# Kernel tuning notes

Measured on AMD Instinct MI355X. Metric: run time of the kernel, lower is better.

The kernel has to match this reference:

```python
import jax, jax.numpy as jnp
import numpy as np

DN = ('NCHW', 'OIHW', 'NCHW')
A, NC = 3, 80  # num_anchors, num_classes


def conv(x, w, b, pad=1):
    y = jax.lax.conv_general_dilated(x, w, (1, 1), [(pad, pad), (pad, pad)], dimension_numbers=DN)
    return y + b[None, :, None, None]


def up2(x):
    return jnp.repeat(jnp.repeat(x, 2, axis=2), 2, axis=3)


def gen_anchors():
    # AnchorGenerator: sizes per level, 3 aspect ratios, 1 scale, stride=2**(i+3)
    sizes = [32.0, 64.0, 128.0]
    ars = [0.5, 1.0, 2.0]
    hw = [(64, 64), (32, 32), (16, 16)]
    out = []
    for i, ((h, w), bs) in enumerate(zip(hw, sizes)):
        stride = 2.0 ** (i + 3)
        base = np.array([[-bs * np.sqrt(a) / 2, -bs / np.sqrt(a) / 2,
                          bs * np.sqrt(a) / 2, bs / np.sqrt(a) / 2] for a in ars], dtype=np.float32)
        sx = np.arange(w, dtype=np.float32) * stride
        sy = np.arange(h, dtype=np.float32) * stride
        yy, xx = np.meshgrid(sy, sx, indexing='ij')  # torch.meshgrid default 'ij'
        shifts = np.stack([xx.ravel(), yy.ravel(), xx.ravel(), yy.ravel()], axis=1)
        anc = (base[None, :, :] + shifts[:, None, :]).reshape(-1, 4)
        out.append(anc)
    return jnp.asarray(np.concatenate(out, axis=0))


def setup_inputs() -> dict:
    key = jax.random.key(0)
    ks = jax.random.split(key, 32)
    def w(k, o, i, kh, kw):
        return jax.random.normal(k, (o, i, kh, kw), jnp.float32) * 0.02
    B = 8
    inp = {
        'feat3': jax.random.normal(ks[0], (B, 512, 64, 64), jnp.float32),
        'feat4': jax.random.normal(ks[1], (B, 1024, 32, 32), jnp.float32),
        'feat5': jax.random.normal(ks[2], (B, 2048, 16, 16), jnp.float32),
        # FPN lateral 1x1 convs
        'lw0': w(ks[3], 256, 512, 1, 1),  'lb0': jnp.zeros(256, jnp.float32),
        'lw1': w(ks[4], 256, 1024, 1, 1), 'lb1': jnp.zeros(256, jnp.float32),
        'lw2': w(ks[5], 256, 2048, 1, 1), 'lb2': jnp.zeros(256, jnp.float32),
        # FPN 3x3 output convs
        'fw0': w(ks[6], 256, 256, 3, 3), 'fb0': jnp.zeros(256, jnp.float32),
        'fw1': w(ks[7], 256, 256, 3, 3), 'fb1': jnp.zeros(256, jnp.float32),
        'fw2': w(ks[8], 256, 256, 3, 3), 'fb2': jnp.zeros(256, jnp.float32),
        # cls tower (shared across levels)
        'cw0': w(ks[9], 256, 256, 3, 3),  'cb0': jnp.zeros(256, jnp.float32),
        'cw1': w(ks[10], 256, 256, 3, 3), 'cb1': jnp.zeros(256, jnp.float32),
        'cw2': w(ks[11], A * NC, 256, 3, 3), 'cb2': jnp.zeros(A * NC, jnp.float32),
        # reg tower (shared across levels)
        'rw0': w(ks[12], 256, 256, 3, 3), 'rb0': jnp.zeros(256, jnp.float32),
        'rw1': w(ks[13], 256, 256, 3, 3), 'rb1': jnp.zeros(256, jnp.float32),
        'rw2': w(ks[14], A * 4, 256, 3, 3), 'rb2': jnp.zeros(A * 4, jnp.float32),
    }
    return inp


def _tower(f, w0, b0, w1, b1, w2, b2):
    x = jax.nn.relu(conv(f, w0, b0))
    x = jax.nn.relu(conv(x, w1, b1))
    return conv(x, w2, b2)


def reference(feat3, feat4, feat5,
              lw0, lb0, lw1, lb1, lw2, lb2,
              fw0, fb0, fw1, fb1, fw2, fb2,
              cw0, cb0, cw1, cb1, cw2, cb2,
              rw0, rb0, rw1, rb1, rw2, rb2):
    B = feat3.shape[0]
    # FPN: lateral 1x1 convs + top-down nearest upsample fusion + 3x3 convs
    l0 = conv(feat3, lw0, lb0, pad=0)
    l1 = conv(feat4, lw1, lb1, pad=0)
    l2 = conv(feat5, lw2, lb2, pad=0)
    l1 = l1 + up2(l2)
    l0 = l0 + up2(l1)
    feats = [conv(l0, fw0, fb0), conv(l1, fw1, fb1), conv(l2, fw2, fb2)]
    cls_list, reg_list = [], []
    for f in feats:
        c = _tower(f, cw0, cb0, cw1, cb1, cw2, cb2)  # [B, A*NC, H, W]
        r = _tower(f, rw0, rb0, rw1, rb1, rw2, rb2)  # [B, A*4, H, W]
        H, W = c.shape[2], c.shape[3]
        # view(B, A, C, HW).permute(0, 3, 1, 2) -> [B, HW, A, C]
        c = c.reshape(B, A, NC, H * W).transpose(0, 3, 1, 2)
        r = r.reshape(B, A, 4, H * W).transpose(0, 3, 1, 2)
        cls_list.append(c.reshape(B, H * W, A * NC))
        reg_list.append(r.reshape(B, H * W, A * 4))
    cls_all = jnp.concatenate(cls_list, axis=1)   # [B, 5376, 240]
    reg_all = jnp.concatenate(reg_list, axis=1)   # [B, 5376, 12]
    out = jnp.concatenate([cls_all, reg_all], axis=-1)  # [B, 5376, 252]
    anchors = gen_anchors()  # [16128, 4]
    return out, anchors
```

## Files before the change

### kernel.cpp

```cpp
#include <hip/hip_runtime.h>

typedef __bf16 bf16_t;
typedef __bf16 bf16x8 __attribute__((ext_vector_type(8)));
typedef float f32x4 __attribute__((ext_vector_type(4)));

__device__ inline void gl_lds16(const bf16_t* g, bf16_t* l) {
  __builtin_amdgcn_global_load_lds(
      (const __attribute__((address_space(1))) void*)g,
      (__attribute__((address_space(3))) void*)l, 16, 0, 0);
}

__global__ __launch_bounds__(256)
void nchw_to_nhwc(const float* __restrict__ in, bf16_t* __restrict__ out,
                  int C, int HW) {
  __shared__ float tile[64][65];
  const int n = blockIdx.z;
  const int c0 = blockIdx.y * 64, p0 = blockIdx.x * 64;
  const int t = threadIdx.x;
  const float* src = in + ((size_t)n * C + c0) * HW + p0;
  const int cl = t >> 6;
  const int pl = t & 63;
#pragma unroll
  for (int i = 0; i < 16; ++i)
    tile[cl + i * 4][pl] = src[(size_t)(cl + i * 4) * HW + pl];
  __syncthreads();
  bf16_t* dst = out + ((size_t)n * HW + p0) * C + c0;
  const int pc = t >> 6;
  const int cc = t & 63;
#pragma unroll
  for (int i = 0; i < 16; ++i)
    dst[(size_t)(pc + i * 4) * C + cc] = (bf16_t)tile[cc][pc + i * 4];
}

struct WSrc {
  const float *lw0, *lw1, *lw2;
  const float* w9[9];
  int O9[9];
};
__global__ __launch_bounds__(256)
void weight_prep(WSrc s, bf16_t* __restrict__ LWT0, bf16_t* __restrict__ LWT1,
                 bf16_t* __restrict__ LWT2, bf16_t* __restrict__ W33) {
  int idx = blockIdx.x * 256 + threadIdx.x;
  if (idx < 131072) { LWT0[idx] = (bf16_t)s.lw0[idx]; return; }
  if (idx < 393216) { int i = idx - 131072; LWT1[i] = (bf16_t)s.lw1[i]; return; }
  if (idx < 917504) { int i = idx - 393216; LWT2[i] = (bf16_t)s.lw2[i]; return; }
  int t2 = idx - 917504;
  if (t2 >= 9 * 589824) return;
  int sgi = t2 / 589824;
  int r = t2 - sgi * 589824;
  int kid = r >> 16;
  int rem = r & 65535;
  int o = rem >> 8, ci = rem & 255;
  const float* src = s.w9[sgi];
  int O = s.O9[sgi];
  W33[t2] = (o < O) ? (bf16_t)src[((size_t)o * 256 + ci) * 9 + kid] : (bf16_t)0.0f;
}

__global__ __launch_bounds__(256)
void up2_add_p(bf16_t* __restrict__ dst, const bf16_t* __restrict__ src,
               int lw, int lhw, int dWp, int dNs, int sWp, int sNs, int tot8) {
  int idx = blockIdx.x * 256 + threadIdx.x;
  if (idx >= tot8) return;
  const int c8 = idx & 31;
  const int pos = idx >> 5;
  const int n = pos >> lhw;
  const int rem = pos & ((1 << lhw) - 1);
  const int y = rem >> lw, x = rem & ((1 << lw) - 1);
  bf16_t* d = dst + ((size_t)n * dNs + (y + 1) * dWp + (x + 1)) * 256 + c8 * 8;
  const bf16_t* sp = src + ((size_t)n * sNs + ((y >> 1) + 1) * sWp + ((x >> 1) + 1)) * 256 + c8 * 8;
  bf16x8 dv = *(bf16x8*)d;
  bf16x8 sv = *(const bf16x8*)sp;
#pragma unroll
  for (int k = 0; k < 8; ++k) dv[k] = (bf16_t)((float)dv[k] + (float)sv[k]);
  *(bf16x8*)d = dv;
}

struct Job {
  const bf16_t* A;
  const bf16_t* Wt;
  const float* bias;
  bf16_t* outb;
  int mtiles, ntiles;
  int lw, lhw;
  int Wp, nsA;
  int oWp, onstride;
  int Cin, nk, relu, Cout, pos_off, ch_off, use_outf, pad_;
};
struct JobPack { Job j[6]; };

__global__ __launch_bounds__(256, 2)
void conv_batch(JobPack jp, float* __restrict__ outf) {
  __shared__ __align__(16) bf16_t As[128 * 32];
  __shared__ __align__(16) bf16_t Bs[128 * 32];
  int b = blockIdx.x, ji = 0;
#pragma unroll 1
  for (; ji < 5; ++ji) {
    int sz = jp.j[ji].mtiles * jp.j[ji].ntiles;
    if (b < sz) break;
    b -= sz;
  }
  const Job J = jp.j[ji];
  const int nt = (J.ntiles == 2) ? (b & 1) : 0;
  const int mt = (J.ntiles == 2) ? (b >> 1) : b;
  const int m0 = mt * 128, n0 = nt * 128;
  const int t = threadIdx.x, l = t & 63, w = t >> 6;
  const int W = 1 << J.lw, HW = 1 << J.lhw;

  const int sr = l >> 2, seg = (l & 3) * 8;
  const bf16_t* aptr[2];
  const bf16_t* bptr[2];
  bf16_t* alds[2];
  bf16_t* blds[2];
#pragma unroll
  for (int q = 0; q < 2; ++q) {
    const int r = w * 32 + q * 16 + sr;
    const int mA = m0 + r;
    const int n = mA >> J.lhw;
    const int hw = mA & (HW - 1);
    const int y = hw >> J.lw, x = hw & (W - 1);
    aptr[q] = J.A + ((size_t)n * J.nsA + y * J.Wp + x) * J.Cin + seg;
    alds[q] = &As[(w * 32 + q * 16) * 32];
    const int co = n0 + w * 32 + q * 16 + sr;
    bptr[q] = J.Wt + (size_t)co * J.Cin + seg;
    blds[q] = &Bs[(w * 32 + q * 16) * 32];
  }

  const int fr = l & 15, qd = l >> 4;
  const int wm = (w & 1) * 64, wn = (w >> 1) * 64;

  f32x4 acc[4][4];
#pragma unroll
  for (int i = 0; i < 4; ++i)
#pragma unroll
    for (int j = 0; j < 4; ++j)
#pragma unroll
      for (int r = 0; r < 4; ++r) acc[i][j][r] = 0.0f;

  const int cinb = J.Cin >> 5;
  const int kiters = J.nk * cinb;
  const int colA = J.Cin - (cinb - 1) * 32;
  const int rowA = (J.Wp - 2) * J.Cin - (cinb - 1) * 32;
  const int wrapB = 256 * J.Cin - (cinb - 1) * 32;
  int cb = 0, kid = 0;

#pragma unroll 1
  for (int kk = 0; kk < kiters; ++kk) {
    __syncthreads();
    gl_lds16(aptr[0], alds[0]);
    gl_lds16(aptr[1], alds[1]);
    gl_lds16(bptr[0], blds[0]);
    gl_lds16(bptr[1], blds[1]);
    __syncthreads();
    int dA = 32, dB = 32;
    if (++cb == cinb) {
      cb = 0; ++kid;
      dB = wrapB;
      dA = ((kid == 3) | (kid == 6)) ? rowA : colA;
    }
    aptr[0] += dA; aptr[1] += dA; bptr[0] += dB; bptr[1] += dB;

    bf16x8 af[4], bfv[4];
#pragma unroll
    for (int i = 0; i < 4; ++i)
      af[i] = *(const bf16x8*)&As[(wm + i * 16 + fr) * 32 + qd * 8];
#pragma unroll
    for (int j = 0; j < 4; ++j)
      bfv[j] = *(const bf16x8*)&Bs[(wn + j * 16 + fr) * 32 + qd * 8];
#pragma unroll
    for (int i = 0; i < 4; ++i)
#pragma unroll
      for (int j = 0; j < 4; ++j)
        acc[i][j] = __builtin_amdgcn_mfma_f32_16x16x32_bf16(af[i], bfv[j],
                                                            acc[i][j], 0, 0, 0);
  }

#pragma unroll
  for (int i = 0; i < 4; ++i) {
    const int mrow = m0 + wm + i * 16 + qd * 4;
#pragma unroll
    for (int j = 0; j < 4; ++j) {
      const int co = n0 + wn + j * 16 + fr;
      if (co < J.Cout) {
        const float bv = J.bias[co];
#pragma unroll
        for (int r = 0; r < 4; ++r) {
          float v = acc[i][j][r] + bv;
          if (J.relu) v = fmaxf(v, 0.0f);
          const int m = mrow + r;
          const int n = m >> J.lhw, hw = m & (HW - 1);
          if (J.use_outf) {
            outf[((size_t)n * 5376 + J.pos_off + hw) * 252 + J.ch_off + co] = v;
          } else {
            const int y = hw >> J.lw, x = hw & (W - 1);
            J.outb[((size_t)n * J.onstride + (y + 1) * J.oWp + (x + 1)) * 256 + co] =
                (bf16_t)v;
          }
        }
      }
    }
  }
}

__global__ __launch_bounds__(256)
void anchors_k(float* __restrict__ out) {
  int r = blockIdx.x * 256 + threadIdx.x;
  if (r >= 16128) return;
  int local, w, stride;
  float bs;
  if (r < 12288)      { local = r;          w = 64; stride = 8;  bs = 32.f;  }
  else if (r < 15360) { local = r - 12288;  w = 32; stride = 16; bs = 64.f;  }
  else                { local = r - 15360;  w = 16; stride = 32; bs = 128.f; }
  const int a = local % 3;
  const int s = local / 3;
  const int y = s / w, x = s - y * w;
  const float ar = (a == 0) ? 0.5f : (a == 1) ? 1.0f : 2.0f;
  const float sq = sqrtf(ar);
  const float hw_ = bs * sq * 0.5f, hh = bs / sq * 0.5f;
  const float cx = (float)x * (float)stride, cy = (float)y * (float)stride;
  out[(size_t)r * 4 + 0] = cx - hw_;
  out[(size_t)r * 4 + 1] = cy - hh;
  out[(size_t)r * 4 + 2] = cx + hw_;
  out[(size_t)r * 4 + 3] = cy + hh;
}

extern "C" void kernel_launch(void* const* d_in, const int* in_sizes, int n_in,
                              void* d_out, int out_size, void* d_ws, size_t ws_size,
                              hipStream_t stream) {
  const float* feat3 = (const float*)d_in[0];
  const float* feat4 = (const float*)d_in[1];
  const float* feat5 = (const float*)d_in[2];
  const float* lw0 = (const float*)d_in[3];  const float* lb0 = (const float*)d_in[4];
  const float* lw1 = (const float*)d_in[5];  const float* lb1 = (const float*)d_in[6];
  const float* lw2 = (const float*)d_in[7];  const float* lb2 = (const float*)d_in[8];
  const float* fw0 = (const float*)d_in[9];  const float* fb0 = (const float*)d_in[10];
  const float* fw1 = (const float*)d_in[11]; const float* fb1 = (const float*)d_in[12];
  const float* fw2 = (const float*)d_in[13]; const float* fb2 = (const float*)d_in[14];
  const float* cw0 = (const float*)d_in[15]; const float* cb0 = (const float*)d_in[16];
  const float* cw1 = (const float*)d_in[17]; const float* cb1 = (const float*)d_in[18];
  const float* cw2 = (const float*)d_in[19]; const float* cb2 = (const float*)d_in[20];
  const float* rw0 = (const float*)d_in[21]; const float* rb0 = (const float*)d_in[22];
  const float* rw1 = (const float*)d_in[23]; const float* rb1 = (const float*)d_in[24];
  const float* rw2 = (const float*)d_in[25]; const float* rb2 = (const float*)d_in[26];

  char* ws = (char*)d_ws;
  float* out = (float*)d_out;

  bf16_t* XS3 = (bf16_t*)(ws + 0);
  bf16_t* XS4 = (bf16_t*)(ws + 33554432);
  bf16_t* XS5 = (bf16_t*)(ws + 50331648);
  bf16_t* Lp0 = (bf16_t*)(ws + 58720256);
  bf16_t* Lp1 = (bf16_t*)(ws + 76562432);
  bf16_t* Lp2 = (bf16_t*)(ws + 81297408);
  bf16_t* Pp0 = (bf16_t*)(ws + 82624512);
  bf16_t* Pp1 = (bf16_t*)(ws + 100466688);
  bf16_t* Pp2 = (bf16_t*)(ws + 105201664);
  bf16_t* LWT0 = (bf16_t*)(ws + 106528768);
  bf16_t* LWT1 = (bf16_t*)(ws + 106790912);
  bf16_t* LWT2 = (bf16_t*)(ws + 107315200);
  bf16_t* W33  = (bf16_t*)(ws + 108363776);
  bf16_t* FWT0 = W33 + 0 * 589824;
  bf16_t* FWT1 = W33 + 1 * 589824;
  bf16_t* FWT2 = W33 + 2 * 589824;
  bf16_t* CWT0 = W33 + 3 * 589824;
  bf16_t* CWT1 = W33 + 4 * 589824;
  bf16_t* CWT2 = W33 + 5 * 589824;
  bf16_t* RWT0 = W33 + 6 * 589824;
  bf16_t* RWT1 = W33 + 7 * 589824;
  bf16_t* RWT2 = W33 + 8 * 589824;
  bf16_t* TAc0 = (bf16_t*)(ws + 0);
  bf16_t* TAr0 = (bf16_t*)(ws + 17842176);
  bf16_t* TAc1 = (bf16_t*)(ws + 35684352);
  bf16_t* TAr1 = (bf16_t*)(ws + 40419328);
  bf16_t* TAc2 = (bf16_t*)(ws + 45154304);
  bf16_t* TAr2 = (bf16_t*)(ws + 46481408);
  bf16_t* TBc0 = Pp0; bf16_t* TBr0 = Lp0;
  bf16_t* TBc1 = Pp1; bf16_t* TBr1 = Lp1;
  bf16_t* TBc2 = Pp2; bf16_t* TBr2 = Lp2;

  WSrc wsrc;
  wsrc.lw0 = lw0; wsrc.lw1 = lw1; wsrc.lw2 = lw2;
  const float* w9s[9] = {fw0, fw1, fw2, cw0, cw1, cw2, rw0, rw1, rw2};
  int o9s[9] = {256, 256, 256, 256, 256, 240, 256, 256, 12};
  for (int i = 0; i < 9; ++i) { wsrc.w9[i] = w9s[i]; wsrc.O9[i] = o9s[i]; }
  weight_prep<<<dim3(24320), 256, 0, stream>>>(wsrc, LWT0, LWT1, LWT2, W33);

  nchw_to_nhwc<<<dim3(64, 8, 8),  256, 0, stream>>>(feat3, XS3, 512, 4096);
  nchw_to_nhwc<<<dim3(16, 16, 8), 256, 0, stream>>>(feat4, XS4, 1024, 1024);
  nchw_to_nhwc<<<dim3(4, 32, 8),  256, 0, stream>>>(feat5, XS5, 2048, 256);

  hipMemsetAsync(ws + 58720256, 0, 47808512, stream);

  auto mkjob = [](const bf16_t* A, const bf16_t* Wt, const float* bias,
                  bf16_t* outb, int mtiles, int ntiles, int lw, int lhw,
                  int Wp, int nsA, int oWp, int onstride, int Cin, int nk,
                  int relu, int Cout, int pos_off, int ch_off, int use_outf) {
    Job j;
    j.A = A; j.Wt = Wt; j.bias = bias; j.outb = outb;
    j.mtiles = mtiles; j.ntiles = ntiles; j.lw = lw; j.lhw = lhw;
    j.Wp = Wp; j.nsA = nsA; j.oWp = oWp; j.onstride = onstride;
    j.Cin = Cin; j.nk = nk; j.relu = relu; j.Cout = Cout;
    j.pos_off = pos_off; j.ch_off = ch_off; j.use_outf = use_outf; j.pad_ = 0;
    return j;
  };

  {
    JobPack jp;
    jp.j[0] = mkjob(XS3, LWT0, lb0, Lp0, 256, 2, 6, 12, 64, 4096, 66, 4356, 512, 1, 0, 256, 0, 0, 0);
    jp.j[1] = mkjob(XS4, LWT1, lb1, Lp1, 64, 2, 5, 10, 32, 1024, 34, 1156, 1024, 1, 0, 256, 0, 0, 0);
    jp.j[2] = mkjob(XS5, LWT2, lb2, Lp2, 16, 2, 4, 8, 16, 256, 18, 324, 2048, 1, 0, 256, 0, 0, 0);
    jp.j[3] = jp.j[4] = jp.j[5] = jp.j[2]; jp.j[3].mtiles = jp.j[4].mtiles = jp.j[5].mtiles = 0;
    conv_batch<<<dim3(672), 256, 0, stream>>>(jp, out);
  }

  hipMemsetAsync(ws + 0, 0, 47808512, stream);

  up2_add_p<<<dim3(1024), 256, 0, stream>>>(Lp1, Lp2, 5, 10, 34, 1156, 18, 324, 262144);
  up2_add_p<<<dim3(4096), 256, 0, stream>>>(Lp0, Lp1, 6, 12, 66, 4356, 34, 1156, 1048576);

  {
    JobPack jp;
    jp.j[0] = mkjob(Lp0, FWT0, fb0, Pp0, 256, 2, 6, 12, 66, 4356, 66, 4356, 256, 9, 0, 256, 0, 0, 0);
    jp.j[1] = mkjob(Lp1, FWT1, fb1, Pp1, 64, 2, 5, 10, 34, 1156, 34, 1156, 256, 9, 0, 256, 0, 0, 0);
    jp.j[2] = mkjob(Lp2, FWT2, fb2, Pp2, 16, 2, 4, 8, 18, 324, 18, 324, 256, 9, 0, 256, 0, 0, 0);
    jp.j[3] = jp.j[4] = jp.j[5] = jp.j[2]; jp.j[3].mtiles = jp.j[4].mtiles = jp.j[5].mtiles = 0;
    conv_batch<<<dim3(672), 256, 0, stream>>>(jp, out);
  }

  {
    JobPack jp;
    jp.j[0] = mkjob(Pp0, CWT0, cb0, TAc0, 256, 2, 6, 12, 66, 4356, 66, 4356, 256, 9, 1, 256, 0, 0, 0);
    jp.j[1] = mkjob(Pp0, RWT0, rb0, TAr0, 256, 2, 6, 12, 66, 4356, 66, 4356, 256, 9, 1, 256, 0, 0, 0);
    jp.j[2] = mkjob(Pp1, CWT0, cb0, TAc1, 64, 2, 5, 10, 34, 1156, 34, 1156, 256, 9, 1, 256, 0, 0, 0);
    jp.j[3] = mkjob(Pp1, RWT0, rb0, TAr1, 64, 2, 5, 10, 34, 1156, 34, 1156, 256, 9, 1, 256, 0, 0, 0);
    jp.j[4] = mkjob(Pp2, CWT0, cb0, TAc2, 16, 2, 4, 8, 18, 324, 18, 324, 256, 9, 1, 256, 0, 0, 0);
    jp.j[5] = mkjob(Pp2, RWT0, rb0, TAr2, 16, 2, 4, 8, 18, 324, 18, 324, 256, 9, 1, 256, 0, 0, 0);
    conv_batch<<<dim3(1344), 256, 0, stream>>>(jp, out);
  }

  {
    JobPack jp;
    jp.j[0] = mkjob(TAc0, CWT1, cb1, TBc0, 256, 2, 6, 12, 66, 4356, 66, 4356, 256, 9, 1, 256, 0, 0, 0);
    jp.j[1] = mkjob(TAr0, RWT1, rb1, TBr0, 256, 2, 6, 12, 66, 4356, 66, 4356, 256, 9, 1, 256, 0, 0, 0);
    jp.j[2] = mkjob(TAc1, CWT1, cb1, TBc1, 64, 2, 5, 10, 34, 1156, 34, 1156, 256, 9, 1, 256, 0, 0, 0);
    jp.j[3] = mkjob(TAr1, RWT1, rb1, TBr1, 64, 2, 5, 10, 34, 1156, 34, 1156, 256, 9, 1, 256, 0, 0, 0);
    jp.j[4] = mkjob(TAc2, CWT1, cb1, TBc2, 16, 2, 4, 8, 18, 324, 18, 324, 256, 9, 1, 256, 0, 0, 0);
    jp.j[5] = mkjob(TAr2, RWT1, rb1, TBr2, 16, 2, 4, 8, 18, 324, 18, 324, 256, 9, 1, 256, 0, 0, 0);
    conv_batch<<<dim3(1344), 256, 0, stream>>>(jp, out);
  }

  {
    JobPack jp;
    jp.j[0] = mkjob(TBc0, CWT2, cb2, nullptr, 256, 2, 6, 12, 66, 4356, 0, 0, 256, 9, 0, 240, 0, 0, 1);
    jp.j[1] = mkjob(TBr0, RWT2, rb2, nullptr, 256, 1, 6, 12, 66, 4356, 0, 0, 256, 9, 0, 12, 0, 240, 1);
    jp.j[2] = mkjob(TBc1, CWT2, cb2, nullptr, 64, 2, 5, 10, 34, 1156, 0, 0, 256, 9, 0, 240, 4096, 0, 1);
    jp.j[3] = mkjob(TBr1, RWT2, rb2, nullptr, 64, 1, 5, 10, 34, 1156, 0, 0, 256, 9, 0, 12, 4096, 240, 1);
    jp.j[4] = mkjob(TBc2, CWT2, cb2, nullptr, 16, 2, 4, 8, 18, 324, 0, 0, 256, 9, 0, 240, 5120, 0, 1);
    jp.j[5] = mkjob(TBr2, RWT2, rb2, nullptr, 16, 1, 4, 8, 18, 324, 0, 0, 256, 9, 0, 12, 5120, 240, 1);
    conv_batch<<<dim3(1008), 256, 0, stream>>>(jp, out);
  }

  anchors_k<<<dim3(63), 256, 0, stream>>>(out + 10838016);
}
```

Measured before the change: 772.0 us.

## Stage padded input halo tile in LDS once per channel block for 3x3 convs

Splits the generic conv kernel into a specialized 1x1 kernel and a new 3x3 kernel. The 3x3 kernel loads the padded halo rows of the input tile into LDS once per 32-channel block and reuses them for all nine taps, instead of re-fetching the A tile from global memory for every tap. It also loads three taps of weights per sync step, cutting the number of barriers. This raises LDS usage to about 44 KB per block and changes occupancy hints, so fewer blocks may fit per CU.

```diff
diff --git a/kernel.cpp b/kernel.cpp
--- a/kernel.cpp
+++ b/kernel.cpp
@@ -75,37 +75,31 @@
   *(bf16x8*)d = dv;
 }
 
-struct Job {
+struct Job1 {
   const bf16_t* A;
   const bf16_t* Wt;
   const float* bias;
   bf16_t* outb;
-  int mtiles, ntiles;
-  int lw, lhw;
-  int Wp, nsA;
-  int oWp, onstride;
-  int Cin, nk, relu, Cout, pos_off, ch_off, use_outf, pad_;
+  int mtiles, lw, lhw, oWp, onstride, Cin, pad0, pad1;
 };
-struct JobPack { Job j[6]; };
+struct Job1Pack { Job1 j[3]; };
 
 __global__ __launch_bounds__(256, 2)
-void conv_batch(JobPack jp, float* __restrict__ outf) {
+void conv1_batch(Job1Pack jp) {
   __shared__ __align__(16) bf16_t As[128 * 32];
   __shared__ __align__(16) bf16_t Bs[128 * 32];
   int b = blockIdx.x, ji = 0;
 #pragma unroll 1
-  for (; ji < 5; ++ji) {
-    int sz = jp.j[ji].mtiles * jp.j[ji].ntiles;
+  for (; ji < 2; ++ji) {
+    int sz = jp.j[ji].mtiles * 2;
     if (b < sz) break;
     b -= sz;
   }
-  const Job J = jp.j[ji];
-  const int nt = (J.ntiles == 2) ? (b & 1) : 0;
-  const int mt = (J.ntiles == 2) ? (b >> 1) : b;
+  const Job1 J = jp.j[ji];
+  const int nt = b & 1, mt = b >> 1;
   const int m0 = mt * 128, n0 = nt * 128;
   const int t = threadIdx.x, l = t & 63, w = t >> 6;
   const int W = 1 << J.lw, HW = 1 << J.lhw;
-
   const int sr = l >> 2, seg = (l & 3) * 8;
   const bf16_t* aptr[2];
   const bf16_t* bptr[2];
@@ -114,17 +108,11 @@
 #pragma unroll
   for (int q = 0; q < 2; ++q) {
     const int r = w * 32 + q * 16 + sr;
-    const int mA = m0 + r;
-    const int n = mA >> J.lhw;
-    const int hw = mA & (HW - 1);
-    const int y = hw >> J.lw, x = hw & (W - 1);
-    aptr[q] = J.A + ((size_t)n * J.nsA + y * J.Wp + x) * J.Cin + seg;
+    aptr[q] = J.A + (size_t)(m0 + r) * J.Cin + seg;
     alds[q] = &As[(w * 32 + q * 16) * 32];
-    const int co = n0 + w * 32 + q * 16 + sr;
-    bptr[q] = J.Wt + (size_t)co * J.Cin + seg;
+    bptr[q] = J.Wt + (size_t)(n0 + r) * J.Cin + seg;
     blds[q] = &Bs[(w * 32 + q * 16) * 32];
   }
-
   const int fr = l & 15, qd = l >> 4;
   const int wm = (w & 1) * 64, wn = (w >> 1) * 64;
 
@@ -136,13 +124,7 @@
 #pragma unroll
       for (int r = 0; r < 4; ++r) acc[i][j][r] = 0.0f;
 
-  const int cinb = J.Cin >> 5;
-  const int kiters = J.nk * cinb;
-  const int colA = J.Cin - (cinb - 1) * 32;
-  const int rowA = (J.Wp - 2) * J.Cin - (cinb - 1) * 32;
-  const int wrapB = 256 * J.Cin - (cinb - 1) * 32;
-  int cb = 0, kid = 0;
-
+  const int kiters = J.Cin >> 5;
 #pragma unroll 1
   for (int kk = 0; kk < kiters; ++kk) {
     __syncthreads();
@@ -151,14 +133,7 @@
     gl_lds16(bptr[0], blds[0]);
     gl_lds16(bptr[1], blds[1]);
     __syncthreads();
-    int dA = 32, dB = 32;
-    if (++cb == cinb) {
-      cb = 0; ++kid;
-      dB = wrapB;
-      dA = ((kid == 3) | (kid == 6)) ? rowA : colA;
-    }
-    aptr[0] += dA; aptr[1] += dA; bptr[0] += dB; bptr[1] += dB;
-
+    aptr[0] += 32; aptr[1] += 32; bptr[0] += 32; bptr[1] += 32;
     bf16x8 af[4], bfv[4];
 #pragma unroll
     for (int i = 0; i < 4; ++i)
@@ -172,6 +147,122 @@
       for (int j = 0; j < 4; ++j)
         acc[i][j] = __builtin_amdgcn_mfma_f32_16x16x32_bf16(af[i], bfv[j],
                                                             acc[i][j], 0, 0, 0);
+  }
+
+#pragma unroll
+  for (int i = 0; i < 4; ++i) {
+    const int mrow = m0 + wm + i * 16 + qd * 4;
+#pragma unroll
+    for (int j = 0; j < 4; ++j) {
+      const int co = n0 + wn + j * 16 + fr;
+      const float bv = J.bias[co];
+#pragma unroll
+      for (int r = 0; r < 4; ++r) {
+        float v = acc[i][j][r] + bv;
+        const int m = mrow + r;
+        const int n = m >> J.lhw, hw = m & (HW - 1);
+        const int y = hw >> J.lw, x = hw & (W - 1);
+        J.outb[((size_t)n * J.onstride + (y + 1) * J.oWp + (x + 1)) * 256 + co] =
+            (bf16_t)v;
+      }
+    }
+  }
+}
+
+struct Job3 {
+  const bf16_t* A;
+  const bf16_t* Wt;
+  const float* bias;
+  bf16_t* outb;
+  int mtiles, ntiles, lw, lhw, Wp, nsA, oWp, onstride;
+  int relu, Cout, pos_off, ch_off, use_outf, nAr, Pc, pad_;
+};
+struct Job3Pack { Job3 j[6]; };
+
+__global__ __launch_bounds__(256, 3)
+void conv3_batch(Job3Pack jp, float* __restrict__ outf) {
+  __shared__ __align__(16) bf16_t As[320 * 32];
+  __shared__ __align__(16) bf16_t Bs[384 * 32];
+  int b = blockIdx.x, ji = 0;
+#pragma unroll 1
+  for (; ji < 5; ++ji) {
+    int sz = jp.j[ji].mtiles * jp.j[ji].ntiles;
+    if (b < sz) break;
+    b -= sz;
+  }
+  const Job3 J = jp.j[ji];
+  const int nt = (J.ntiles == 2) ? (b & 1) : 0;
+  const int mt = (J.ntiles == 2) ? (b >> 1) : b;
+  const int m0 = mt * 128, n0 = nt * 128;
+  const int t = threadIdx.x, l = t & 63, w = t >> 6;
+  const int W = 1 << J.lw, HW = 1 << J.lhw;
+  const int sr = l >> 2, seg = (l & 3) * 8;
+  const int fr = l & 15, qd = l >> 4;
+  const int wm = (w & 1) * 64, wn = (w >> 1) * 64;
+
+  const int n_img = m0 >> J.lhw;
+  const int Y0 = (m0 & (HW - 1)) >> J.lw;
+  const bf16_t* Ag = J.A + ((size_t)n_img * J.nsA + (size_t)Y0 * J.Wp) * 256;
+
+  int apix[4];
+#pragma unroll
+  for (int i = 0; i < 4; ++i) {
+    const int m = wm + i * 16 + fr;
+    const int y = m >> J.lw, x = m & (W - 1);
+    apix[i] = ((y + 1) * J.Wp + (x + 1)) * 32 + qd * 8;
+  }
+
+  f32x4 acc[4][4];
+#pragma unroll
+  for (int i = 0; i < 4; ++i)
+#pragma unroll
+    for (int j = 0; j < 4; ++j)
+#pragma unroll
+      for (int r = 0; r < 4; ++r) acc[i][j][r] = 0.0f;
+
+#pragma unroll 1
+  for (int cb = 0; cb < 8; ++cb) {
+    const int cboff = cb * 32;
+#pragma unroll 1
+    for (int ky = 0; ky < 3; ++ky) {
+      __syncthreads();
+#pragma unroll
+      for (int r = 0; r < 6; ++r) {
+        const int R = r * 64 + w * 16 + sr;
+        const int tp = R >> 7, co = R & 127;
+        gl_lds16(J.Wt + (size_t)(ky * 3 + tp) * 65536 +
+                     (size_t)(n0 + co) * 256 + cboff + seg,
+                 &Bs[(r * 64 + w * 16) * 32]);
+      }
+      if (ky == 0) {
+#pragma unroll 1
+        for (int r = 0; r < J.nAr; ++r) {
+          int p = r * 64 + w * 16 + sr;
+          p = (p < J.Pc) ? p : (J.Pc - 1);
+          gl_lds16(Ag + (size_t)p * 256 + cboff + seg,
+                   &As[(r * 64 + w * 16) * 32]);
+        }
+      }
+      __syncthreads();
+      const int dyoff = (ky - 1) * J.Wp * 32;
+#pragma unroll
+      for (int kx = 0; kx < 3; ++kx) {
+        const int d = dyoff + (kx - 1) * 32;
+        bf16x8 af[4], bfv[4];
+#pragma unroll
+        for (int i = 0; i < 4; ++i)
+          af[i] = *(const bf16x8*)&As[apix[i] + d];
+#pragma unroll
+        for (int j = 0; j < 4; ++j)
+          bfv[j] = *(const bf16x8*)&Bs[(kx * 128 + wn + j * 16 + fr) * 32 + qd * 8];
+#pragma unroll
+        for (int i = 0; i < 4; ++i)
+#pragma unroll
+          for (int j = 0; j < 4; ++j)
+            acc[i][j] = __builtin_amdgcn_mfma_f32_16x16x32_bf16(af[i], bfv[j],
+                                                                acc[i][j], 0, 0, 0);
+      }
+    }
   }
 
 #pragma unroll
@@ -290,73 +381,73 @@
 
   hipMemsetAsync(ws + 58720256, 0, 47808512, stream);
 
-  auto mkjob = [](const bf16_t* A, const bf16_t* Wt, const float* bias,
-                  bf16_t* outb, int mtiles, int ntiles, int lw, int lhw,
-                  int Wp, int nsA, int oWp, int onstride, int Cin, int nk,
-                  int relu, int Cout, int pos_off, int ch_off, int use_outf) {
-    Job j;
+  {
+    Job1Pack jp;
+    jp.j[0] = {XS3, LWT0, lb0, Lp0, 256, 6, 12, 66, 4356, 512, 0, 0};
+    jp.j[1] = {XS4, LWT1, lb1, Lp1, 64, 5, 10, 34, 1156, 1024, 0, 0};
+    jp.j[2] = {XS5, LWT2, lb2, Lp2, 16, 4, 8, 18, 324, 2048, 0, 0};
+    conv1_batch<<<dim3(672), 256, 0, stream>>>(jp);
+  }
+
+  hipMemsetAsync(ws + 0, 0, 47808512, stream);
+
+  up2_add_p<<<dim3(1024), 256, 0, stream>>>(Lp1, Lp2, 5, 10, 34, 1156, 18, 324, 262144);
+  up2_add_p<<<dim3(4096), 256, 0, stream>>>(Lp0, Lp1, 6, 12, 66, 4356, 34, 1156, 1048576);
+
+  auto mk3 = [](const bf16_t* A, const bf16_t* Wt, const float* bias,
+                bf16_t* outb, int mtiles, int ntiles, int lw, int lhw,
+                int Wp, int nsA, int oWp, int onstride, int relu, int Cout,
+                int pos_off, int ch_off, int use_outf, int nAr, int Pc) {
+    Job3 j;
     j.A = A; j.Wt = Wt; j.bias = bias; j.outb = outb;
     j.mtiles = mtiles; j.ntiles = ntiles; j.lw = lw; j.lhw = lhw;
     j.Wp = Wp; j.nsA = nsA; j.oWp = oWp; j.onstride = onstride;
-    j.Cin = Cin; j.nk = nk; j.relu = relu; j.Cout = Cout;
-    j.pos_off = pos_off; j.ch_off = ch_off; j.use_outf = use_outf; j.pad_ = 0;
+    j.relu = relu; j.Cout = Cout; j.pos_off = pos_off; j.ch_off = ch_off;
+    j.use_outf = use_outf; j.nAr = nAr; j.Pc = Pc; j.pad_ = 0;
     return j;
   };
 
   {
-    JobPack jp;
-    jp.j[0] = mkjob(XS3, LWT0, lb0, Lp0, 256, 2, 6, 12, 64, 4096, 66, 4356, 512, 1, 0, 256, 0, 0, 0);
-    jp.j[1] = mkjob(XS4, LWT1, lb1, Lp1, 64, 2, 5, 10, 32, 1024, 34, 1156, 1024, 1, 0, 256, 0, 0, 0);
-    jp.j[2] = mkjob(XS5, LWT2, lb2, Lp2, 16, 2, 4, 8, 16, 256, 18, 324, 2048, 1, 0, 256, 0, 0, 0);
-    jp.j[3] = jp.j[4] = jp.j[5] = jp.j[2]; jp.j[3].mtiles = jp.j[4].mtiles = jp.j[5].mtiles = 0;
-    conv_batch<<<dim3(672), 256, 0, stream>>>(jp, out);
-  }
-
-  hipMemsetAsync(ws + 0, 0, 47808512, stream);
-
-  up2_add_p<<<dim3(1024), 256, 0, stream>>>(Lp1, Lp2, 5, 10, 34, 1156, 18, 324, 262144);
-  up2_add_p<<<dim3(4096), 256, 0, stream>>>(Lp0, Lp1, 6, 12, 66, 4356, 34, 1156, 1048576);
+    Job3Pack jp;
+    jp.j[0] = mk3(Lp0, FWT0, fb0, Pp0, 256, 2, 6, 12, 66, 4356, 66, 4356, 0, 256, 0, 0, 0, 5, 264);
+    jp.j[1] = mk3(Lp1, FWT1, fb1, Pp1, 64, 2, 5, 10, 34, 1156, 34, 1156, 0, 256, 0, 0, 0, 4, 204);
+    jp.j[2] = mk3(Lp2, FWT2, fb2, Pp2, 16, 2, 4, 8, 18, 324, 18, 324, 0, 256, 0, 0, 0, 3, 180);
+    jp.j[3] = jp.j[4] = jp.j[5] = jp.j[2];
+    jp.j[3].mtiles = jp.j[4].mtiles = jp.j[5].mtiles = 0;
+    conv3_batch<<<dim3(672), 256, 0, stream>>>(jp, out);
+  }
 
   {
-    JobPack jp;
-    jp.j[0] = mkjob(Lp0, FWT0, fb0, Pp0, 256, 2, 6, 12, 66, 4356, 66, 4356, 256, 9, 0, 256, 0, 0, 0);
-    jp.j[1] = mkjob(Lp1, FWT1, fb1, Pp1, 64, 2, 5, 10, 34, 1156, 34, 1156, 256, 9, 0, 256, 0, 0, 0);
-    jp.j[2] = mkjob(Lp2, FWT2, fb2, Pp2, 16, 2, 4, 8, 18, 324, 18, 324, 256, 9, 0, 256, 0, 0, 0);
-    jp.j[3] = jp.j[4] = jp.j[5] = jp.j[2]; jp.j[3].mtiles = jp.j[4].mtiles = jp.j[5].mtiles = 0;
-    conv_batch<<<dim3(672), 256, 0, stream>>>(jp, out);
+    Job3Pack jp;
+    jp.j[0] = mk3(Pp0, CWT0, cb0, TAc0, 256, 2, 6, 12, 66, 4356, 66, 4356, 1, 256, 0, 0, 0, 5, 264);
+    jp.j[1] = mk3(Pp0, RWT0, rb0, TAr0, 256, 2, 6, 12, 66, 4356, 66, 4356, 1, 256, 0, 0, 0, 5, 264);
+    jp.j[2] = mk3(Pp1, CWT0, cb0, TAc1, 64, 2, 5, 10, 34, 1156, 34, 1156, 1, 256, 0, 0, 0, 4, 204);
+    jp.j[3] = mk3(Pp1, RWT0, rb0, TAr1, 64, 2, 5, 10, 34, 1156, 34, 1156, 1, 256, 0, 0, 0, 4, 204);
+    jp.j[4] = mk3(Pp2, CWT0, cb0, TAc2, 16, 2, 4, 8, 18, 324, 18, 324, 1, 256, 0, 0, 0, 3, 180);
+    jp.j[5] = mk3(Pp2, RWT0, rb0, TAr2, 16, 2, 4, 8, 18, 324, 18, 324, 1, 256, 0, 0, 0, 3, 180);
+    conv3_batch<<<dim3(1344), 256, 0, stream>>>(jp, out);
   }
 
   {
-    JobPack jp;
-    jp.j[0] = mkjob(Pp0, CWT0, cb0, TAc0, 256, 2, 6, 12, 66, 4356, 66, 4356, 256, 9, 1, 256, 0, 0, 0);
-    jp.j[1] = mkjob(Pp0, RWT0, rb0, TAr0, 256, 2, 6, 12, 66, 4356, 66, 4356, 256, 9, 1, 256, 0, 0, 0);
-    jp.j[2] = mkjob(Pp1, CWT0, cb0, TAc1, 64, 2, 5, 10, 34, 1156, 34, 1156, 256, 9, 1, 256, 0, 0, 0);
-    jp.j[3] = mkjob(Pp1, RWT0, rb0, TAr1, 64, 2, 5, 10, 34, 1156, 34, 1156, 256, 9, 1, 256, 0, 0, 0);
-    jp.j[4] = mkjob(Pp2, CWT0, cb0, TAc2, 16, 2, 4, 8, 18, 324, 18, 324, 256, 9, 1, 256, 0, 0, 0);
-    jp.j[5] = mkjob(Pp2, RWT0, rb0, TAr2, 16, 2, 4, 8, 18, 324, 18, 324, 256, 9, 1, 256, 0, 0, 0);
-    conv_batch<<<dim3(1344), 256, 0, stream>>>(jp, out);
+    Job3Pack jp;
+    jp.j[0] = mk3(TAc0, CWT1, cb1, TBc0, 256, 2, 6, 12, 66, 4356, 66, 4356, 1, 256, 0, 0, 0, 5, 264);
+    jp.j[1] = mk3(TAr0, RWT1, rb1, TBr0, 256, 2, 6, 12, 66, 4356, 66, 4356, 1, 256, 0, 0, 0, 5, 264);
+    jp.j[2] = mk3(TAc1, CWT1, cb1, TBc1, 64, 2, 5, 10, 34, 1156, 34, 1156, 1, 256, 0, 0, 0, 4, 204);
+    jp.j[3] = mk3(TAr1, RWT1, rb1, TBr1, 64, 2, 5, 10, 34, 1156, 34, 1156, 1, 256, 0, 0, 0, 4, 204);
+    jp.j[4] = mk3(TAc2, CWT1, cb1, TBc2, 16, 2, 4, 8, 18, 324, 18, 324, 1, 256, 0, 0, 0, 3, 180);
+    jp.j[5] = mk3(TAr2, RWT1, rb1, TBr2, 16, 2, 4, 8, 18, 324, 18, 324, 1, 256, 0, 0, 0, 3, 180);
+    conv3_batch<<<dim3(1344), 256, 0, stream>>>(jp, out);
   }
 
   {
-    JobPack jp;
-    jp.j[0] = mkjob(TAc0, CWT1, cb1, TBc0, 256, 2, 6, 12, 66, 4356, 66, 4356, 256, 9, 1, 256, 0, 0, 0);
-    jp.j[1] = mkjob(TAr0, RWT1, rb1, TBr0, 256, 2, 6, 12, 66, 4356, 66, 4356, 256, 9, 1, 256, 0, 0, 0);
-    jp.j[2] = mkjob(TAc1, CWT1, cb1, TBc1, 64, 2, 5, 10, 34, 1156, 34, 1156, 256, 9, 1, 256, 0, 0, 0);
-    jp.j[3] = mkjob(TAr1, RWT1, rb1, TBr1, 64, 2, 5, 10, 34, 1156, 34, 1156, 256, 9, 1, 256, 0, 0, 0);
-    jp.j[4] = mkjob(TAc2, CWT1, cb1, TBc2, 16, 2, 4, 8, 18, 324, 18, 324, 256, 9, 1, 256, 0, 0, 0);
-    jp.j[5] = mkjob(TAr2, RWT1, rb1, TBr2, 16, 2, 4, 8, 18, 324, 18, 324, 256, 9, 1, 256, 0, 0, 0);
-    conv_batch<<<dim3(1344), 256, 0, stream>>>(jp, out);
-  }
-
-  {
-    JobPack jp;
-    jp.j[0] = mkjob(TBc0, CWT2, cb2, nullptr, 256, 2, 6, 12, 66, 4356, 0, 0, 256, 9, 0, 240, 0, 0, 1);
-    jp.j[1] = mkjob(TBr0, RWT2, rb2, nullptr, 256, 1, 6, 12, 66, 4356, 0, 0, 256, 9, 0, 12, 0, 240, 1);
-    jp.j[2] = mkjob(TBc1, CWT2, cb2, nullptr, 64, 2, 5, 10, 34, 1156, 0, 0, 256, 9, 0, 240, 4096, 0, 1);
-    jp.j[3] = mkjob(TBr1, RWT2, rb2, nullptr, 64, 1, 5, 10, 34, 1156, 0, 0, 256, 9, 0, 12, 4096, 240, 1);
-    jp.j[4] = mkjob(TBc2, CWT2, cb2, nullptr, 16, 2, 4, 8, 18, 324, 0, 0, 256, 9, 0, 240, 5120, 0, 1);
-    jp.j[5] = mkjob(TBr2, RWT2, rb2, nullptr, 16, 1, 4, 8, 18, 324, 0, 0, 256, 9, 0, 12, 5120, 240, 1);
-    conv_batch<<<dim3(1008), 256, 0, stream>>>(jp, out);
+    Job3Pack jp;
+    jp.j[0] = mk3(TBc0, CWT2, cb2, nullptr, 256, 2, 6, 12, 66, 4356, 0, 0, 0, 240, 0, 0, 1, 5, 264);
+    jp.j[1] = mk3(TBr0, RWT2, rb2, nullptr, 256, 1, 6, 12, 66, 4356, 0, 0, 0, 12, 0, 240, 1, 5, 264);
+    jp.j[2] = mk3(TBc1, CWT2, cb2, nullptr, 64, 2, 5, 10, 34, 1156, 0, 0, 0, 240, 4096, 0, 1, 4, 204);
+    jp.j[3] = mk3(TBr1, RWT2, rb2, nullptr, 64, 1, 5, 10, 34, 1156, 0, 0, 0, 12, 4096, 240, 1, 4, 204);
+    jp.j[4] = mk3(TBc2, CWT2, cb2, nullptr, 16, 2, 4, 8, 18, 324, 0, 0, 0, 240, 5120, 0, 1, 3, 180);
+    jp.j[5] = mk3(TBr2, RWT2, rb2, nullptr, 16, 1, 4, 8, 18, 324, 0, 0, 0, 12, 5120, 240, 1, 3, 180);
+    conv3_batch<<<dim3(1008), 256, 0, stream>>>(jp, out);
   }
 
   anchors_k<<<dim3(63), 256, 0, stream>>>(out + 10838016);
```

After: 664.2 us. 1.16x faster.
